# Kernel optimization log

Measured on AMD Instinct MI355X. Metric: run time of the kernel, lower is better.

Reference implementation:

```python
import jax, jax.numpy as jnp
import numpy as np

N, E, IN, HID, HEADS, K = 50000, 800000, 7, 64, 4, 4


def _add_self_loops(src, dst, edge_attr, n):
    # PyG add_self_loops with fill_value='mean': loop attr = mean of incoming edge attrs per node
    ones = jnp.ones((src.shape[0],), edge_attr.dtype)
    cnt = jax.ops.segment_sum(ones, dst, num_segments=n)
    loop_attr = jax.ops.segment_sum(edge_attr, dst, num_segments=n) / jnp.maximum(cnt, 1.0)[:, None]
    ar = jnp.arange(n, dtype=src.dtype)
    return (jnp.concatenate([src, ar]), jnp.concatenate([dst, ar]),
            jnp.concatenate([edge_attr, loop_attr], axis=0))


def _gat_conv(x, src, dst, eattr, W, a_src, a_dst, We, a_edge, bias, heads, outc, concat, n):
    xw = (x @ W).reshape(n, heads, outc)                      # [N,H,C]
    al_s = jnp.sum(xw * a_src, -1)                            # [N,H]
    al_d = jnpm if False else jnp.sum(xw * a_dst, -1)         # [N,H]
    ew = (eattr @ We).reshape(-1, heads, outc)                # [E,H,C]
    al_e = jnp.sum(ew * a_edge, -1)                           # [E,H]
    alpha = jax.nn.leaky_relu(al_s[src] + al_d[dst] + al_e, 0.2)
    # segment softmax over incoming edges of each dst node (every node has a self loop)
    m = jax.ops.segment_max(alpha, dst, num_segments=n)
    alpha = jnp.exp(alpha - m[dst])
    denom = jax.ops.segment_sum(alpha, dst, num_segments=n)
    alpha = alpha / (denom[dst] + 1e-16)
    out = jax.ops.segment_sum(xw[src] * alpha[..., None], dst, num_segments=n)  # [N,H,C]
    out = out.reshape(n, heads * outc) if concat else out.mean(axis=1)
    return out + bias


def setup_inputs() -> dict:
    key = jax.random.key(0)
    ks = jax.random.split(key, 24)
    s = lambda d: 1.0 / np.sqrt(d)
    inp = {
        'x': jax.random.uniform(ks[0], (N, IN), jnp.float32),
        'edge_index': jax.random.randint(ks[1], (2, E), 0, N),
        'edge_attr': jax.random.uniform(ks[2], (E, 1), jnp.float32),
        'assignments': jax.random.randint(ks[3], (N,), 0, K),
        # conv1 (heads=4, concat)
        'W1': jax.random.normal(ks[4], (IN, HEADS * HID), jnp.float32) * s(IN),
        'att_src1': jax.random.normal(ks[5], (HEADS, HID), jnp.float32) * s(HID),
        'att_dst1': jax.random.normal(ks[6], (HEADS, HID), jnp.float32) * s(HID),
        'We1': jax.random.normal(ks[7], (1, HEADS * HID), jnp.float32),
        'att_e1': jax.random.normal(ks[8], (HEADS, HID), jnp.float32) * s(HID),
        'b1': jnp.zeros((HEADS * HID,), jnp.float32),
        # conv2 (heads=1, mean)
        'W2': jax.random.normal(ks[9], (HEADS * HID, HID), jnp.float32) * s(HEADS * HID),
        'att_src2': jax.random.normal(ks[10], (1, HID), jnp.float32) * s(HID),
        'att_dst2': jax.random.normal(ks[11], (1, HID), jnp.float32) * s(HID),
        'We2': jax.random.normal(ks[12], (1, HID), jnp.float32),
        'att_e2': jax.random.normal(ks[13], (1, HID), jnp.float32) * s(HID),
        'b2': jnp.zeros((HID,), jnp.float32),
        # actor MLP: Linear(HID+1, HID) -> ReLU -> Linear(HID, 1)
        'A1': jax.random.normal(ks[14], (HID + 1, HID), jnp.float32) * s(HID + 1),
        'c1': jnp.zeros((HID,), jnp.float32),
        'A2': jax.random.normal(ks[15], (HID, 1), jnp.float32) * s(HID),
        'c2': jnp.zeros((1,), jnp.float32),
    }
    return inp


def reference(x, edge_index, edge_attr, assignments,
              W1, att_src1, att_dst1, We1, att_e1, b1,
              W2, att_src2, att_dst2, We2, att_e2, b2,
              A1, c1, A2, c2):
    n = x.shape[0]
    src, dst, ea = _add_self_loops(edge_index[0], edge_index[1], edge_attr, n)
    h = jax.nn.elu(_gat_conv(x, src, dst, ea, W1, att_src1, att_dst1, We1, att_e1, b1,
                             HEADS, HID, True, n))
    h = _gat_conv(h, src, dst, ea, W2, att_src2, att_dst2, We2, att_e2, b2,
                  1, HID, False, n)
    # masked segment-mean pooling over clusters (all K clusters non-empty w.h.p.)
    ones = jnp.ones((n,), h.dtype)
    cnt = jax.ops.segment_sum(ones, assignments, num_segments=K)
    safe = jnp.maximum(cnt, 1.0)
    z = jax.ops.segment_sum(h, assignments, num_segments=K) / safe[:, None]     # [K,HID]
    cf = jax.ops.segment_sum(x[:, 6], assignments, num_segments=K) / safe       # [K]
    nonempty = (cnt > 0)
    z = jnp.where(nonempty[:, None], z, 0.0)
    cf = jnp.where(nonempty, cf, 0.0)
    zcf = jnp.concatenate([z, cf[:, None]], axis=-1)                            # [K,HID+1]
    logits = (jax.nn.relu(zcf @ A1 + c1) @ A2 + c2)[:, 0]                        # [K]
    probs = jax.nn.softmax(logits)[None, :]                                      # [1,K]
    z_flat = z.reshape(1, -1)                                                    # [1,K*HID]
    return probs, z_flat
```

## Files before the change

### kernel.cpp

```cpp
#include <hip/hip_runtime.h>
#include <hip/hip_bf16.h>

#define HEADS 4
#define KCL 4
#define BSHIFT 5
#define BW 32
#define NBUCKMAX 1568
#define BCAP 1024
#define EPT 8
#define NSLICE 8
typedef unsigned long long u64;
typedef short short8 __attribute__((ext_vector_type(8)));
typedef float f32x4 __attribute__((ext_vector_type(4)));

__device__ __forceinline__ unsigned short bf16_rne(float f) {
    unsigned int u = __float_as_uint(f);
    u += 0x7FFFu + ((u >> 16) & 1u);
    return (unsigned short)(u >> 16);
}
__device__ __forceinline__ float bf16_to_f32(unsigned short h) {
    return __uint_as_float(((unsigned int)h) << 16);
}


__global__ __launch_bounds__(256) void k_prep_bin(const float* __restrict__ x,
                                                  const float* __restrict__ W1, const float* __restrict__ W2,
                                                  const float* __restrict__ as1, const float* __restrict__ ad1,
                                                  const float* __restrict__ as2, const float* __restrict__ ad2,
                                                  const float* __restrict__ We1, const float* __restrict__ ae1,
                                                  const float* __restrict__ We2, const float* __restrict__ ae2,
                                                  float* __restrict__ ce1, float* __restrict__ ce2,
                                                  float* __restrict__ u_s, float* __restrict__ u_d,
                                                  unsigned short* __restrict__ W2T,
                                                  float* __restrict__ nrec,
                                                  const int* __restrict__ src, const int* __restrict__ dst,
                                                  const float* __restrict__ ea,
                                                  unsigned int* __restrict__ gtail,
                                                  u64* __restrict__ gbuck,
                                                  int N_, int E_, int NB, int nbuck) {
    int t = threadIdx.x;
    if ((int)blockIdx.x >= NB) {
        __shared__ unsigned int cnt[NBUCKMAX];
        __shared__ unsigned int gb[NBUCKMAX];
        for (int i = t; i < nbuck; i += 256) cnt[i] = 0u;
        __syncthreads();
        int bid = blockIdx.x - NB;
        int e0 = bid * (256 * EPT) + t;
        u64 pk[EPT]; int bk[EPT]; unsigned int ls[EPT];
#pragma unroll
        for (int i = 0; i < EPT; i++) {
            int e = e0 + i * 256;
            bool valid = e < E_;
            int s = 0, d = 0; float a = 0.0f;
            if (valid) { s = src[e]; d = dst[e]; a = ea[e]; }
            int b = d >> BSHIFT;
            int lo = d & (BW - 1);
            pk[i] = ((u64)__float_as_uint(a) << 32) | ((u64)(unsigned int)lo << 24) | (unsigned int)s;
            bk[i] = b;
            ls[i] = valid ? atomicAdd(&cnt[b], 1u) : 0u;
        }
        __syncthreads();
        for (int i = t; i < nbuck; i += 256)
            gb[i] = (cnt[i] > 0u) ? atomicAdd(&gtail[i], cnt[i]) : 0u;
        __syncthreads();
#pragma unroll
        for (int i = 0; i < EPT; i++) {
            if (e0 + i * 256 < E_) {
                unsigned int pos = gb[bk[i]] + ls[i];
                if (pos < BCAP) gbuck[(size_t)bk[i] * BCAP + pos] = pk[i];
            }
        }
        return;
    }
    __shared__ float Ps_l[7][4], Pd_l[7][4];
    int h = t >> 6, lane = t & 63;
    for (int i = 0; i < 7; i++) {
        float a = W1[i * 256 + t];
        float ps = a * as1[t];
        float pd = a * ad1[t];
        for (int off = 32; off; off >>= 1) {
            ps += __shfl_down(ps, off, 64);
            pd += __shfl_down(pd, off, 64);
        }
        if (lane == 0) { Ps_l[i][h] = ps; Pd_l[i][h] = pd; }
    }
    if (blockIdx.x == 0) {
        float p = We1[t] * ae1[t];
        for (int off = 32; off; off >>= 1) p += __shfl_down(p, off, 64);
        if (lane == 0) ce1[h] = p;
        if (t < 64) {
            float q = We2[t] * ae2[t];
            for (int off = 32; off; off >>= 1) q += __shfl_down(q, off, 64);
            if (t == 0) ce2[0] = q;
        }
        float us = 0.f, ud = 0.f;
        const float* wr = W2 + t * 64;
        for (int n = 0; n < 64; n++) { us += wr[n] * as2[n]; ud += wr[n] * ad2[n]; }
        u_s[t] = us; u_d[t] = ud;
    }
    int gidx = blockIdx.x * 256 + t;
    if (gidx < 16384) {
        int nn = gidx & 63, k = gidx >> 6;
        W2T[nn * 256 + k] = bf16_rne(W2[k * 64 + nn]);
    }
    __syncthreads();
    int n = gidx;
    if (n >= N_) return;
    float xv[7];
#pragma unroll
    for (int i = 0; i < 7; i++) xv[i] = x[n * 7 + i];
    float4 als = make_float4(0.f, 0.f, 0.f, 0.f);
    float4 ald = make_float4(0.f, 0.f, 0.f, 0.f);
#pragma unroll
    for (int i = 0; i < 7; i++) {
        als.x += xv[i] * Ps_l[i][0]; als.y += xv[i] * Ps_l[i][1];
        als.z += xv[i] * Ps_l[i][2]; als.w += xv[i] * Ps_l[i][3];
        ald.x += xv[i] * Pd_l[i][0]; ald.y += xv[i] * Pd_l[i][1];
        ald.z += xv[i] * Pd_l[i][2]; ald.w += xv[i] * Pd_l[i][3];
    }
    float4* nr = (float4*)(nrec + (size_t)n * 16);
    nr[0] = als;
    nr[1] = ald;
    nr[2] = make_float4(xv[0], xv[1], xv[2], xv[3]);
    nr[3] = make_float4(xv[4], xv[5], xv[6], 0.0f);
}

__global__ __launch_bounds__(256) void k_agg1_xw2g(const unsigned int* __restrict__ gtail,
                                                   const u64* __restrict__ gbuck,
                                                   u64* __restrict__ gpacked,
                                                   int2* __restrict__ idx2,
                                                   const float* __restrict__ nrec,
                                                   const float* __restrict__ ce1,
                                                   const float* __restrict__ W1,
                                                   const float* __restrict__ b1,
                                                   const unsigned short* __restrict__ W2T,
                                                   const float* __restrict__ u_s,
                                                   const float* __restrict__ u_d,
                                                   unsigned short* __restrict__ xw2b,
                                                   float* __restrict__ al_s2,
                                                   float* __restrict__ al_d2, int N_) {
    __shared__ float Xs2[32][36];
    __shared__ __align__(16) unsigned short A_lds[32][264];
    __shared__ u64 esorted[BCAP];
    __shared__ unsigned int rdeg[32], rstart[32], rcur[32];
    __shared__ float als_p[32], ald_p[32];
    int t = threadIdx.x;
    int b = blockIdx.x;
    int m0 = b * 32;
    size_t base = (size_t)b * BCAP;
    u64* raw = (u64*)&A_lds[0][0];
    unsigned int n = gtail[b]; if (n > BCAP) n = BCAP;
    if (t < 32) rdeg[t] = 0u;
    __syncthreads();
    for (unsigned int pos = t; pos < n; pos += 256) {
        u64 p = __builtin_nontemporal_load(&gbuck[base + pos]);
        raw[pos] = p;
        atomicAdd(&rdeg[(unsigned int)(p >> 24) & 31u], 1u);
    }
    __syncthreads();
    if (t < 32) {
        unsigned int deg = rdeg[t];
        unsigned int inc = deg;
#pragma unroll
        for (int off = 1; off < 32; off <<= 1) {
            unsigned int u = __shfl_up(inc, off, 64);
            if (t >= off) inc += u;
        }
        unsigned int start = inc - deg;
        rstart[t] = start; rcur[t] = start;
        if (m0 + t < N_) idx2[m0 + t] = make_int2((int)(base + start), (int)deg);
    }
    __syncthreads();
    for (unsigned int pos = t; pos < n; pos += 256) {
        u64 p = raw[pos];
        unsigned int slot = atomicAdd(&rcur[(unsigned int)(p >> 24) & 31u], 1u);
        esorted[slot] = p;
    }
    __syncthreads();
    for (unsigned int pos = t; pos < n; pos += 256) gpacked[base + pos] = esorted[pos];
    {
        int dl = t >> 3, d = m0 + dl;
        int sub = t & 7, h = sub >> 1, half = sub & 1;
        bool act = d < N_;
        float4 A = make_float4(0.f, 0.f, 0.f, 0.f);
        float4 B = make_float4(0.f, 0.f, 0.f, 0.f);
        if (act) {
            const u64* row = esorted + rstart[dl];
            int cnt = (int)rdeg[dl];
            const float* nd = nrec + (size_t)d * 16;
            float ald = nd[4 + h];
            float ce = ce1[h];
            float easum = 0.0f;
#define E1(J) { \
            u64 p = row[(J)]; \
            int s = (int)(p & 0xFFFFFFu); \
            float a = __uint_as_float((unsigned int)(p >> 32)); \
            const float* ns = nrec + (size_t)s * 16; \
            float als = ns[h]; \
            float4 xa = *(const float4*)(ns + 8); \
            float4 xb = *(const float4*)(ns + 12); \
            easum += a; \
            float v = als + ald + a * ce; \
            v = v > 0.f ? v : 0.2f * v; \
            float w = __expf(v); \
            A.x += w * xa.x; A.y += w * xa.y; A.z += w * xa.z; A.w += w * xa.w; \
            B.x += w * xb.x; B.y += w * xb.y; B.z += w * xb.z; B.w += w; }
            int j = half;
            for (; j + 6 < cnt; j += 8) { E1(j); E1(j + 2); E1(j + 4); E1(j + 6); }
            for (; j < cnt; j += 2) { E1(j); }
#undef E1
            A.x += __shfl_xor(A.x, 1, 64);
            A.y += __shfl_xor(A.y, 1, 64);
            A.z += __shfl_xor(A.z, 1, 64);
            A.w += __shfl_xor(A.w, 1, 64);
            B.x += __shfl_xor(B.x, 1, 64);
            B.y += __shfl_xor(B.y, 1, 64);
            B.z += __shfl_xor(B.z, 1, 64);
            B.w += __shfl_xor(B.w, 1, 64);
            easum += __shfl_xor(easum, 1, 64);
            if (!half) {
                float a_self = easum / fmaxf((float)cnt, 1.0f);
                float v = nd[h] + ald + a_self * ce;
                v = v > 0.f ? v : 0.2f * v;
                float w = __expf(v);
                float4 xa = *(const float4*)(nd + 8);
                float4 xb = *(const float4*)(nd + 12);
                A.x += w * xa.x; A.y += w * xa.y; A.z += w * xa.z; A.w += w * xa.w;
                B.x += w * xb.x; B.y += w * xb.y; B.z += w * xb.z; B.w += w;
            }
        }
        if (!half) {
            *(float4*)&Xs2[dl][h * 8] = A;
            *(float4*)&Xs2[dl][h * 8 + 4] = B;
        }
    }
    __syncthreads();
    {
        int r = t >> 3;
        int kk = t & 7;
        float ps = 0.f, pd = 0.f;
#pragma unroll
        for (int hh = 0; hh < 4; hh++) {
            float xv[7];
#pragma unroll
            for (int i = 0; i < 7; i++) xv[i] = Xs2[r][hh * 8 + i];
            float rw = 1.0f / (Xs2[r][hh * 8 + 7] + 1e-16f);
#pragma unroll
            for (int q = 0; q < 8; q++) {
                int k = hh * 64 + q * 8 + kk;
                float s = 0.f;
#pragma unroll
                for (int i = 0; i < 7; i++) s += xv[i] * W1[i * 256 + k];
                float v = s * rw + b1[k];
                float a = v > 0.f ? v : (__expf(v) - 1.0f);
                ps += a * u_s[k];
                pd += a * u_d[k];
                A_lds[r][k] = bf16_rne(a);
            }
        }
        ps += __shfl_xor(ps, 1, 64); pd += __shfl_xor(pd, 1, 64);
        ps += __shfl_xor(ps, 2, 64); pd += __shfl_xor(pd, 2, 64);
        ps += __shfl_xor(ps, 4, 64); pd += __shfl_xor(pd, 4, 64);
        if (kk == 0) { als_p[r] = ps; ald_p[r] = pd; }
    }
    __syncthreads();
    {
        int w = t >> 6, lane = t & 63;
        int mm = lane & 15, quad = lane >> 4;
        int n0 = w * 16;
        f32x4 acc0 = {0.f, 0.f, 0.f, 0.f};
        f32x4 acc1 = {0.f, 0.f, 0.f, 0.f};
        const unsigned short* bptr = W2T + (size_t)(n0 + mm) * 256;
#pragma unroll
        for (int step = 0; step < 8; step++) {
            int kf = step * 32 + quad * 8;
            short8 bf = *(const short8*)&bptr[kf];
            short8 af0 = *(const short8*)&A_lds[mm][kf];
            short8 af1 = *(const short8*)&A_lds[16 + mm][kf];
            acc0 = __builtin_amdgcn_mfma_f32_16x16x32_bf16(af0, bf, acc0, 0, 0, 0);
            acc1 = __builtin_amdgcn_mfma_f32_16x16x32_bf16(af1, bf, acc1, 0, 0, 0);
        }
#pragma unroll
        for (int r = 0; r < 4; r++) {
            int row0 = m0 + quad * 4 + r;
            if (row0 < N_) xw2b[(size_t)row0 * 64 + n0 + mm] = bf16_rne(acc0[r]);
            int row1 = row0 + 16;
            if (row1 < N_) xw2b[(size_t)row1 * 64 + n0 + mm] = bf16_rne(acc1[r]);
        }
    }
    if (t < 32 && m0 + t < N_) { al_s2[m0 + t] = als_p[t]; al_d2[m0 + t] = ald_p[t]; }
}

__global__ __launch_bounds__(256) void k_agg2p(const int2* __restrict__ idx2,
                                               const u64* __restrict__ gpacked,
                                               const float* __restrict__ al_s2,
                                               const float* __restrict__ al_d2,
                                               const float* __restrict__ ce2,
                                               const unsigned short* __restrict__ xw2b,
                                               const float* __restrict__ x,
                                               const int* __restrict__ assign,
                                               float* __restrict__ zsumS, int N_) {
    __shared__ float lz[256];
    __shared__ float lc[KCL], lf[KCL];
    int t = threadIdx.x;
    lz[t] = 0.0f;
    if (t < KCL) { lc[t] = 0.0f; lf[t] = 0.0f; }
    __syncthreads();
    int dl = t >> 3, sub = t & 7;
    float ce = ce2[0];
    int d = blockIdx.x * 32 + dl;
    if (d < N_) {
        int2 ix = idx2[d];
        const u64* row = gpacked + ix.x;
        int cnt = ix.y;
        float ald = al_d2[d];
        float acc[8];
#pragma unroll
        for (int f = 0; f < 8; f++) acc[f] = 0.0f;
        float wsum = 0.0f, easum = 0.0f;
        const unsigned short* xcol = xw2b + sub * 8;
#define EDGE2(P) { \
        int s_ = (int)((P) & 0xFFFFFFu); \
        float a_ = __uint_as_float((unsigned int)((P) >> 32)); \
        float als_ = al_s2[s_]; \
        short8 g_ = *(const short8*)&xcol[(size_t)s_ * 64]; \
        easum += a_; \
        float v_ = als_ + ald + a_ * ce; v_ = v_ > 0.f ? v_ : 0.2f * v_; \
        float w_ = __expf(v_); \
        wsum += w_; \
        _Pragma("unroll") \
        for (int f = 0; f < 8; f++) acc[f] += w_ * bf16_to_f32((unsigned short)g_[f]); }
        int j = 0;
        for (; j + 3 < cnt; j += 4) {
            u64 p0 = row[j], p1 = row[j + 1], p2 = row[j + 2], p3 = row[j + 3];
            EDGE2(p0); EDGE2(p1); EDGE2(p2); EDGE2(p3);
        }
        for (; j < cnt; j++) { u64 p0 = row[j]; EDGE2(p0); }
#undef EDGE2
        float a_self = easum / fmaxf((float)cnt, 1.0f);
        float v = al_s2[d] + ald + a_self * ce;
        v = v > 0.f ? v : 0.2f * v;
        float w = __expf(v);
        short8 gd = *(const short8*)&xcol[(size_t)d * 64];
#pragma unroll
        for (int f = 0; f < 8; f++) acc[f] += w * bf16_to_f32((unsigned short)gd[f]);
        wsum += w;
        float rw = 1.0f / (wsum + 1e-16f);
        int a = assign[d];
#pragma unroll
        for (int f = 0; f < 8; f++) atomicAdd(&lz[a * 64 + sub * 8 + f], acc[f] * rw);
        if (sub == 0) {
            atomicAdd(&lc[a], 1.0f);
            atomicAdd(&lf[a], x[d * 7 + 6]);
        }
    }
    __syncthreads();
    float* zs = zsumS + (size_t)(blockIdx.x & (NSLICE - 1)) * 264;
    atomicAdd(&zs[t], lz[t]);
    if (t < KCL) {
        atomicAdd(&zs[256 + t], lc[t]);
        atomicAdd(&zs[260 + t], lf[t]);
    }
}

__global__ __launch_bounds__(256) void k_head(const float* __restrict__ zsumS, const float* __restrict__ b2,
                                              const float* __restrict__ A1, const float* __restrict__ c1,
                                              const float* __restrict__ A2, const float* __restrict__ c2,
                                              float* __restrict__ out) {
    __shared__ float zcf[KCL][65];
    __shared__ float logits[KCL];
    int t = threadIdx.x;
    int k = t >> 6, c = t & 63;
    float zs = 0.0f, cn = 0.0f, cf = 0.0f;
#pragma unroll
    for (int s = 0; s < NSLICE; s++) {
        const float* sl = zsumS + (size_t)s * 264;
        zs += sl[k * 64 + c];
        cn += sl[256 + k];
        cf += sl[260 + k];
    }
    float z = (cn > 0.f) ? (zs / fmaxf(cn, 1.0f) + b2[c]) : 0.0f;
    zcf[k][c] = z;
    out[4 + k * 64 + c] = z;
    if (c == 0) zcf[k][64] = (cn > 0.f) ? (cf / fmaxf(cn, 1.0f)) : 0.0f;
    __syncthreads();
    {
        int j = c;
        float acc = 0.0f;
        for (int i = 0; i < 65; i++) acc += zcf[k][i] * A1[i * 64 + j];
        float hr = fmaxf(acc + c1[j], 0.0f);
        float contrib = hr * A2[j];
        for (int off = 32; off; off >>= 1) contrib += __shfl_down(contrib, off, 64);
        if (j == 0) logits[k] = contrib + c2[0];
    }
    __syncthreads();
    if (t == 0) {
        float m = fmaxf(fmaxf(logits[0], logits[1]), fmaxf(logits[2], logits[3]));
        float e0 = expf(logits[0] - m), e1 = expf(logits[1] - m);
        float e2 = expf(logits[2] - m), e3 = expf(logits[3] - m);
        float s = e0 + e1 + e2 + e3;
        out[0] = e0 / s; out[1] = e1 / s; out[2] = e2 / s; out[3] = e3 / s;
    }
}

extern "C" void kernel_launch(void* const* d_in, const int* in_sizes, int n_in,
                              void* d_out, int out_size, void* d_ws, size_t ws_size,
                              hipStream_t stream) {
    const float* x      = (const float*)d_in[0];
    const int*   ei     = (const int*)d_in[1];
    const float* eattr  = (const float*)d_in[2];
    const int*   assign = (const int*)d_in[3];
    const float* W1     = (const float*)d_in[4];
    const float* as1    = (const float*)d_in[5];
    const float* ad1    = (const float*)d_in[6];
    const float* We1    = (const float*)d_in[7];
    const float* ae1    = (const float*)d_in[8];
    const float* b1     = (const float*)d_in[9];
    const float* W2     = (const float*)d_in[10];
    const float* as2    = (const float*)d_in[11];
    const float* ad2    = (const float*)d_in[12];
    const float* We2    = (const float*)d_in[13];
    const float* ae2    = (const float*)d_in[14];
    const float* b2     = (const float*)d_in[15];
    const float* A1     = (const float*)d_in[16];
    const float* c1     = (const float*)d_in[17];
    const float* A2     = (const float*)d_in[18];
    const float* c2     = (const float*)d_in[19];
    float* out = (float*)d_out;

    const int N_ = in_sizes[0] / 7;
    const int E_ = in_sizes[2];
    const int NB = (N_ + 255) / 256;
    const int nbuck = (N_ + BW - 1) >> BSHIFT;
    const int NBBIN = (E_ + 256 * EPT - 1) / (256 * EPT);
    const int* srcA = ei;
    const int* dstA = ei + E_;

    float* ws = (float*)d_ws;
    size_t Nz = (size_t)N_;
    float* nrec    = ws;
    float* al_s2   = nrec + 16 * Nz;
    float* al_d2   = al_s2 + Nz;
    float* ce1     = al_d2 + Nz;
    float* ce2     = ce1 + 4;
    float* zsumS   = ce2 + 4;
    unsigned int* gtail = (unsigned int*)(zsumS + NSLICE * 264);
    float* u_s     = (float*)(gtail + NBUCKMAX);
    float* u_d     = u_s + 256;
    unsigned short* xw2b = (unsigned short*)(u_d + 256);
    uintptr_t pp   = (uintptr_t)(xw2b + 64 * Nz);
    u64* gbuck     = (u64*)((pp + 7) & ~(uintptr_t)7);
    u64* gpacked   = gbuck + (size_t)nbuck * BCAP;
    int2* idx2     = (int2*)(gpacked + (size_t)nbuck * BCAP);
    unsigned short* W2T = (unsigned short*)(idx2 + Nz);

    hipMemsetAsync(zsumS, 0, (size_t)(NSLICE * 264 + NBUCKMAX) * sizeof(float), stream);

    k_prep_bin<<<NB + NBBIN, 256, 0, stream>>>(x, W1, W2, as1, ad1, as2, ad2,
                                               We1, ae1, We2, ae2,
                                               ce1, ce2, u_s, u_d, W2T, nrec,
                                               srcA, dstA, eattr, gtail, gbuck,
                                               N_, E_, NB, nbuck);

    k_agg1_xw2g<<<nbuck, 256, 0, stream>>>(gtail, gbuck, gpacked, idx2, nrec, ce1,
                                           W1, b1, W2T, u_s, u_d,
                                           xw2b, al_s2, al_d2, N_);

    k_agg2p<<<nbuck, 256, 0, stream>>>(idx2, gpacked, al_s2, al_d2, ce2, xw2b,
                                       x, assign, zsumS, N_);

    k_head<<<1, 256, 0, stream>>>(zsumS, b2, A1, c1, A2, c2, out);
}
```

Baseline: 205.0 us.

## Re-sort buckets in layer-2 kernel instead of storing sorted edges globally

The layer-1 aggregation kernel no longer writes per-node sorted edge arrays (gpacked) and index pairs (idx2) to global memory. The layer-2 kernel instead reloads the raw bucket from gbuck and redoes the per-bucket counting sort in shared memory. The binning kernel also doubles edges per thread and rereads src/dst/attr in a second pass rather than keeping them in registers. This trades a global write and read for repeated LDS sorting work and extra shared memory in the second kernel, which may lower occupancy.

```diff
diff --git a/kernel.cpp b/kernel.cpp
--- a/kernel.cpp
+++ b/kernel.cpp
@@ -7,7 +7,7 @@
 #define BW 32
 #define NBUCKMAX 1568
 #define BCAP 1024
-#define EPT 8
+#define EPT 16
 #define NSLICE 8
 typedef unsigned long long u64;
 typedef short short8 __attribute__((ext_vector_type(8)));
@@ -41,33 +41,32 @@
     int t = threadIdx.x;
     if ((int)blockIdx.x >= NB) {
         __shared__ unsigned int cnt[NBUCKMAX];
-        __shared__ unsigned int gb[NBUCKMAX];
+        __shared__ unsigned int cur[NBUCKMAX];
         for (int i = t; i < nbuck; i += 256) cnt[i] = 0u;
         __syncthreads();
         int bid = blockIdx.x - NB;
         int e0 = bid * (256 * EPT) + t;
-        u64 pk[EPT]; int bk[EPT]; unsigned int ls[EPT];
 #pragma unroll
         for (int i = 0; i < EPT; i++) {
             int e = e0 + i * 256;
-            bool valid = e < E_;
-            int s = 0, d = 0; float a = 0.0f;
-            if (valid) { s = src[e]; d = dst[e]; a = ea[e]; }
-            int b = d >> BSHIFT;
-            int lo = d & (BW - 1);
-            pk[i] = ((u64)__float_as_uint(a) << 32) | ((u64)(unsigned int)lo << 24) | (unsigned int)s;
-            bk[i] = b;
-            ls[i] = valid ? atomicAdd(&cnt[b], 1u) : 0u;
+            if (e < E_) atomicAdd(&cnt[dst[e] >> BSHIFT], 1u);
         }
         __syncthreads();
         for (int i = t; i < nbuck; i += 256)
-            gb[i] = (cnt[i] > 0u) ? atomicAdd(&gtail[i], cnt[i]) : 0u;
+            cur[i] = (cnt[i] > 0u) ? atomicAdd(&gtail[i], cnt[i]) : 0u;
         __syncthreads();
 #pragma unroll
         for (int i = 0; i < EPT; i++) {
-            if (e0 + i * 256 < E_) {
-                unsigned int pos = gb[bk[i]] + ls[i];
-                if (pos < BCAP) gbuck[(size_t)bk[i] * BCAP + pos] = pk[i];
+            int e = e0 + i * 256;
+            if (e < E_) {
+                int s = src[e], d = dst[e];
+                float a = ea[e];
+                int b = d >> BSHIFT;
+                int lo = d & (BW - 1);
+                unsigned int pos = atomicAdd(&cur[b], 1u);
+                if (pos < BCAP)
+                    gbuck[(size_t)b * BCAP + pos] =
+                        ((u64)__float_as_uint(a) << 32) | ((u64)(unsigned int)lo << 24) | (unsigned int)s;
             }
         }
         return;
@@ -127,8 +126,6 @@
 
 __global__ __launch_bounds__(256) void k_agg1_xw2g(const unsigned int* __restrict__ gtail,
                                                    const u64* __restrict__ gbuck,
-                                                   u64* __restrict__ gpacked,
-                                                   int2* __restrict__ idx2,
                                                    const float* __restrict__ nrec,
                                                    const float* __restrict__ ce1,
                                                    const float* __restrict__ W1,
@@ -168,7 +165,6 @@
         }
         unsigned int start = inc - deg;
         rstart[t] = start; rcur[t] = start;
-        if (m0 + t < N_) idx2[m0 + t] = make_int2((int)(base + start), (int)deg);
     }
     __syncthreads();
     for (unsigned int pos = t; pos < n; pos += 256) {
@@ -177,7 +173,6 @@
         esorted[slot] = p;
     }
     __syncthreads();
-    for (unsigned int pos = t; pos < n; pos += 256) gpacked[base + pos] = esorted[pos];
     {
         int dl = t >> 3, d = m0 + dl;
         int sub = t & 7, h = sub >> 1, half = sub & 1;
@@ -291,8 +286,8 @@
     if (t < 32 && m0 + t < N_) { al_s2[m0 + t] = als_p[t]; al_d2[m0 + t] = ald_p[t]; }
 }
 
-__global__ __launch_bounds__(256) void k_agg2p(const int2* __restrict__ idx2,
-                                               const u64* __restrict__ gpacked,
+__global__ __launch_bounds__(256) void k_agg2p(const unsigned int* __restrict__ gtail,
+                                               const u64* __restrict__ gbuck,
                                                const float* __restrict__ al_s2,
                                                const float* __restrict__ al_d2,
                                                const float* __restrict__ ce2,
@@ -300,19 +295,50 @@
                                                const float* __restrict__ x,
                                                const int* __restrict__ assign,
                                                float* __restrict__ zsumS, int N_) {
+    __shared__ u64 raw[BCAP];
+    __shared__ u64 esorted[BCAP];
+    __shared__ unsigned int rdeg[32], rstart[32], rcur[32];
     __shared__ float lz[256];
     __shared__ float lc[KCL], lf[KCL];
     int t = threadIdx.x;
+    int b = blockIdx.x;
+    int m0 = b * 32;
+    size_t base = (size_t)b * BCAP;
+    unsigned int n = gtail[b]; if (n > BCAP) n = BCAP;
     lz[t] = 0.0f;
     if (t < KCL) { lc[t] = 0.0f; lf[t] = 0.0f; }
+    if (t < 32) rdeg[t] = 0u;
+    __syncthreads();
+    for (unsigned int pos = t; pos < n; pos += 256) {
+        u64 p = __builtin_nontemporal_load(&gbuck[base + pos]);
+        raw[pos] = p;
+        atomicAdd(&rdeg[(unsigned int)(p >> 24) & 31u], 1u);
+    }
+    __syncthreads();
+    if (t < 32) {
+        unsigned int deg = rdeg[t];
+        unsigned int inc = deg;
+#pragma unroll
+        for (int off = 1; off < 32; off <<= 1) {
+            unsigned int u = __shfl_up(inc, off, 64);
+            if (t >= off) inc += u;
+        }
+        unsigned int start = inc - deg;
+        rstart[t] = start; rcur[t] = start;
+    }
+    __syncthreads();
+    for (unsigned int pos = t; pos < n; pos += 256) {
+        u64 p = raw[pos];
+        unsigned int slot = atomicAdd(&rcur[(unsigned int)(p >> 24) & 31u], 1u);
+        esorted[slot] = p;
+    }
     __syncthreads();
     int dl = t >> 3, sub = t & 7;
     float ce = ce2[0];
-    int d = blockIdx.x * 32 + dl;
+    int d = m0 + dl;
     if (d < N_) {
-        int2 ix = idx2[d];
-        const u64* row = gpacked + ix.x;
-        int cnt = ix.y;
+        const u64* row = esorted + rstart[dl];
+        int cnt = (int)rdeg[dl];
         float ald = al_d2[d];
         float acc[8];
 #pragma unroll
@@ -355,7 +381,7 @@
         }
     }
     __syncthreads();
-    float* zs = zsumS + (size_t)(blockIdx.x & (NSLICE - 1)) * 264;
+    float* zs = zsumS + (size_t)(b & (NSLICE - 1)) * 264;
     atomicAdd(&zs[t], lz[t]);
     if (t < KCL) {
         atomicAdd(&zs[256 + t], lc[t]);
@@ -450,9 +476,7 @@
     unsigned short* xw2b = (unsigned short*)(u_d + 256);
     uintptr_t pp   = (uintptr_t)(xw2b + 64 * Nz);
     u64* gbuck     = (u64*)((pp + 7) & ~(uintptr_t)7);
-    u64* gpacked   = gbuck + (size_t)nbuck * BCAP;
-    int2* idx2     = (int2*)(gpacked + (size_t)nbuck * BCAP);
-    unsigned short* W2T = (unsigned short*)(idx2 + Nz);
+    unsigned short* W2T = (unsigned short*)(gbuck + (size_t)nbuck * BCAP);
 
     hipMemsetAsync(zsumS, 0, (size_t)(NSLICE * 264 + NBUCKMAX) * sizeof(float), stream);
 
@@ -462,11 +486,11 @@
                                                srcA, dstA, eattr, gtail, gbuck,
                                                N_, E_, NB, nbuck);
 
-    k_agg1_xw2g<<<nbuck, 256, 0, stream>>>(gtail, gbuck, gpacked, idx2, nrec, ce1,
+    k_agg1_xw2g<<<nbuck, 256, 0, stream>>>(gtail, gbuck, nrec, ce1,
                                            W1, b1, W2T, u_s, u_d,
                                            xw2b, al_s2, al_d2, N_);
 
-    k_agg2p<<<nbuck, 256, 0, stream>>>(idx2, gpacked, al_s2, al_d2, ce2, xw2b,
+    k_agg2p<<<nbuck, 256, 0, stream>>>(gtail, gbuck, al_s2, al_d2, ce2, xw2b,
                                        x, assign, zsumS, N_);
 
     k_head<<<1, 256, 0, stream>>>(zsumS, b2, A1, c1, A2, c2, out);
```

New measurement: 205.6 us. No clear change (+0.3%).
